# Performance work log

Measured on AMD Instinct MI355X. Metric: run time of the kernel, lower is better.

## Reference

```python
import jax, jax.numpy as jnp
import numpy as np

RNN = 50
FEAT = 128
NCLS = 8
ALPHA = 0.3  # keras LeakyReLU default


def setup_inputs() -> dict:
    key = jax.random.key(0)
    ks = jax.random.split(key, 6)
    B, T = 256, 2048
    x = jax.random.normal(ks[0], (B, T, FEAT), dtype=jnp.float32)
    # GRU params (Keras layout: kernel [F,3H], recurrent [H,3H], bias [2,3H] for reset_after=True)
    W = jax.random.normal(ks[1], (FEAT, 3 * RNN), dtype=jnp.float32) / np.sqrt(FEAT)
    U = jax.random.normal(ks[2], (RNN, 3 * RNN), dtype=jnp.float32) / np.sqrt(RNN)
    b = jax.random.normal(ks[3], (2, 3 * RNN), dtype=jnp.float32) * 0.01
    W2 = jax.random.normal(ks[4], (RNN, NCLS), dtype=jnp.float32) / np.sqrt(RNN)
    b2 = jnp.zeros((NCLS,), dtype=jnp.float32)
    return {"inputs": x, "W": W, "U": U, "b": b, "W2": W2, "b2": b2}


def _gru_last_state(x, W, U, b):
    # x: [B,T,F] -> precompute input projections [T,B,3H]
    B = x.shape[0]
    xw = jnp.einsum("btf,fh->tbh", x, W) + b[0]
    h0 = jnp.zeros((B, RNN), dtype=x.dtype)

    def step(h, xt):
        inner = h @ U + b[1]                       # [B,3H]
        z = jax.nn.sigmoid(xt[:, :RNN] + inner[:, :RNN])
        r = jax.nn.sigmoid(xt[:, RNN:2 * RNN] + inner[:, RNN:2 * RNN])
        hh = jnp.tanh(xt[:, 2 * RNN:] + r * inner[:, 2 * RNN:])
        h_new = z * h + (1.0 - z) * hh
        return h_new, None

    h_last, _ = jax.lax.scan(step, h0, xw)
    return h_last  # [B,H]


def reference(inputs, W, U, b, W2, b2):
    h = _gru_last_state(inputs, W, U, b)
    h = jnp.where(h >= 0, h, ALPHA * h)            # LeakyReLU(0.3)
    logits = h @ W2 + b2
    return jax.nn.softmax(logits, axis=-1)
```

## Files before the change

kernel.cpp:

```cpp
#include <hip/hip_runtime.h>

typedef __attribute__((ext_vector_type(4))) float f32x4;
typedef _Float16 f16;
typedef __attribute__((ext_vector_type(2))) _Float16 f16x2;
typedef __attribute__((ext_vector_type(8))) _Float16 f16x8;

#define T_LEN 2048
#define B_SZ 256
#define FEATN 128
#define H 50
#define H3 150
#define XW_STRIDE 160

__device__ __forceinline__ float rcpf(float x) { return __builtin_amdgcn_rcpf(x); }

__device__ __forceinline__ float dot2f(f16x2 a, f16x2 b, float c) {
  return __builtin_amdgcn_fdot2(a, b, c, false);
}

__global__ __launch_bounds__(256) void xw_gemm(const float* __restrict__ x,
                                               const float* __restrict__ W,
                                               f16* __restrict__ xw) {
  __shared__ f16 Wt[160 * 136];
  const int tid = threadIdx.x;
  for (int idx = tid; idx < FEATN * H3; idx += 256) {
    int f = idx / H3;
    int n = idx - f * H3;
    Wt[n * 136 + f] = (f16)W[idx];
  }
  for (int idx = tid; idx < 10 * FEATN; idx += 256) {
    int n = H3 + (idx >> 7);
    int f = idx & 127;
    Wt[n * 136 + f] = (f16)0.f;
  }
  __syncthreads();

  const int wid = tid >> 6;
  const int lane = tid & 63;
  const int l15 = lane & 15;
  const int g = lane >> 4;
  const long row0 = (long)blockIdx.x * 128 + wid * 32;

  f16x8 a[2][4];
#pragma unroll
  for (int sub = 0; sub < 2; ++sub) {
    const float* xp = x + (row0 + sub * 16 + l15) * FEATN + g * 8;
#pragma unroll
    for (int kk = 0; kk < 4; ++kk) {
      f32x4 p0 = *(const f32x4*)(xp + kk * 32);
      f32x4 p1 = *(const f32x4*)(xp + kk * 32 + 4);
      f16x8 v;
      v[0] = (f16)p0[0]; v[1] = (f16)p0[1]; v[2] = (f16)p0[2]; v[3] = (f16)p0[3];
      v[4] = (f16)p1[0]; v[5] = (f16)p1[1]; v[6] = (f16)p1[2]; v[7] = (f16)p1[3];
      a[sub][kk] = v;
    }
  }

  for (int nt = 0; nt < 10; ++nt) {
    const f16* bp = &Wt[(nt * 16 + l15) * 136 + g * 8];
    f16x8 bf0 = *(const f16x8*)(bp);
    f16x8 bf1 = *(const f16x8*)(bp + 32);
    f16x8 bf2 = *(const f16x8*)(bp + 64);
    f16x8 bf3 = *(const f16x8*)(bp + 96);
    f32x4 acc0 = {0.f, 0.f, 0.f, 0.f};
    f32x4 acc1 = {0.f, 0.f, 0.f, 0.f};
    acc0 = __builtin_amdgcn_mfma_f32_16x16x32_f16(a[0][0], bf0, acc0, 0, 0, 0);
    acc0 = __builtin_amdgcn_mfma_f32_16x16x32_f16(a[0][1], bf1, acc0, 0, 0, 0);
    acc0 = __builtin_amdgcn_mfma_f32_16x16x32_f16(a[0][2], bf2, acc0, 0, 0, 0);
    acc0 = __builtin_amdgcn_mfma_f32_16x16x32_f16(a[0][3], bf3, acc0, 0, 0, 0);
    acc1 = __builtin_amdgcn_mfma_f32_16x16x32_f16(a[1][0], bf0, acc1, 0, 0, 0);
    acc1 = __builtin_amdgcn_mfma_f32_16x16x32_f16(a[1][1], bf1, acc1, 0, 0, 0);
    acc1 = __builtin_amdgcn_mfma_f32_16x16x32_f16(a[1][2], bf2, acc1, 0, 0, 0);
    acc1 = __builtin_amdgcn_mfma_f32_16x16x32_f16(a[1][3], bf3, acc1, 0, 0, 0);
    int col = nt * 16 + l15;
    if (col < H3) {
#pragma unroll
      for (int r = 0; r < 4; ++r) {
        long rowA = row0 + g * 4 + r;
        xw[rowA * XW_STRIDE + col] = (f16)acc0[r];
        xw[(rowA + 16) * XW_STRIDE + col] = (f16)acc1[r];
      }
    }
  }
}

__global__ __launch_bounds__(64, 1) void gru_head64(const f16* __restrict__ xw,
                                                    const float* __restrict__ U,
                                                    const float* __restrict__ bias,
                                                    const float* __restrict__ W2,
                                                    const float* __restrict__ b2,
                                                    float* __restrict__ out) {
  __shared__ __align__(16) f16 h_lds16[64];
  __shared__ float fin[52];
  __shared__ float red[8];
  const int l = threadIdx.x;
  const int b = blockIdx.x;
  const int lc = l < H ? l : H - 1;
  const bool act = l < H;
  const long base = (long)b * T_LEN * XW_STRIDE;

  f16x2 uz2[25], ur2[25], uh2[25];
#pragma unroll
  for (int c = 0; c < 25; ++c) {
    uz2[c][0] = (f16)U[(2 * c) * H3 + lc];
    uz2[c][1] = (f16)U[(2 * c + 1) * H3 + lc];
    ur2[c][0] = (f16)U[(2 * c) * H3 + H + lc];
    ur2[c][1] = (f16)U[(2 * c + 1) * H3 + H + lc];
    uh2[c][0] = (f16)U[(2 * c) * H3 + 2 * H + lc];
    uh2[c][1] = (f16)U[(2 * c + 1) * H3 + 2 * H + lc];
  }
  const float bz = bias[lc] + bias[H3 + lc];
  const float br = bias[H + lc] + bias[H3 + H + lc];
  const float b0h = bias[2 * H + lc];
  const float b1h = bias[H3 + 2 * H + lc];

  float hreg = 0.f;
  h_lds16[l] = (f16)0.f;

  const f16* q = xw + base + lc;
  f16 pz[4], pr[4], ph[4];
#pragma unroll
  for (int p = 0; p < 4; ++p) {
    pz[p] = q[p * XW_STRIDE];
    pr[p] = q[p * XW_STRIDE + H];
    ph[p] = q[p * XW_STRIDE + 2 * H];
  }

  const f16x8* hp8 = (const f16x8*)h_lds16;

#define STEP(P, PF)                                                           \
    {                                                                         \
           \
      f16x8 w0 = hp8[0], w1 = hp8[1], w2 = hp8[2];                            \
      f16x8 w3 = hp8[3], w4 = hp8[4], w5 = hp8[5];                            \
      f16x2 w6 = *(const f16x2*)(h_lds16 + 48);                               \
               \
      float xzf = (float)pz[P];                                               \
      float xrf = (float)pr[P];                                               \
      float xhf = (float)ph[P];                                               \
      if (PF) {                                                               \
        pz[P] = q[(P + 4) * XW_STRIDE];                                       \
        pr[P] = q[(P + 4) * XW_STRIDE + H];                                   \
        ph[P] = q[(P + 4) * XW_STRIDE + 2 * H];                               \
      }                                                                       \
      f16x2 hv[25];                                                           \
      hv[0] = __builtin_shufflevector(w0, w0, 0, 1);                          \
      hv[1] = __builtin_shufflevector(w0, w0, 2, 3);                          \
      hv[2] = __builtin_shufflevector(w0, w0, 4, 5);                          \
      hv[3] = __builtin_shufflevector(w0, w0, 6, 7);                          \
      hv[4] = __builtin_shufflevector(w1, w1, 0, 1);                          \
      hv[5] = __builtin_shufflevector(w1, w1, 2, 3);                          \
      hv[6] = __builtin_shufflevector(w1, w1, 4, 5);                          \
      hv[7] = __builtin_shufflevector(w1, w1, 6, 7);                          \
      hv[8] = __builtin_shufflevector(w2, w2, 0, 1);                          \
      hv[9] = __builtin_shufflevector(w2, w2, 2, 3);                          \
      hv[10] = __builtin_shufflevector(w2, w2, 4, 5);                         \
      hv[11] = __builtin_shufflevector(w2, w2, 6, 7);                         \
      hv[12] = __builtin_shufflevector(w3, w3, 0, 1);                         \
      hv[13] = __builtin_shufflevector(w3, w3, 2, 3);                         \
      hv[14] = __builtin_shufflevector(w3, w3, 4, 5);                         \
      hv[15] = __builtin_shufflevector(w3, w3, 6, 7);                         \
      hv[16] = __builtin_shufflevector(w4, w4, 0, 1);                         \
      hv[17] = __builtin_shufflevector(w4, w4, 2, 3);                         \
      hv[18] = __builtin_shufflevector(w4, w4, 4, 5);                         \
      hv[19] = __builtin_shufflevector(w4, w4, 6, 7);                         \
      hv[20] = __builtin_shufflevector(w5, w5, 0, 1);                         \
      hv[21] = __builtin_shufflevector(w5, w5, 2, 3);                         \
      hv[22] = __builtin_shufflevector(w5, w5, 4, 5);                         \
      hv[23] = __builtin_shufflevector(w5, w5, 6, 7);                         \
      hv[24] = w6;                                                            \
      float sz0 = bz, sr0 = br, sh0 = b1h;                                    \
      float sz1 = 0.f, sr1 = 0.f, sh1 = 0.f;                                  \
      _Pragma("unroll")                                                       \
      for (int p = 0; p < 25; ++p) {                                          \
        if (p & 1) {                                                          \
          sz1 = dot2f(hv[p], uz2[p], sz1);                                    \
          sr1 = dot2f(hv[p], ur2[p], sr1);                                    \
          sh1 = dot2f(hv[p], uh2[p], sh1);                                    \
        } else {                                                              \
          sz0 = dot2f(hv[p], uz2[p], sz0);                                    \
          sr0 = dot2f(hv[p], ur2[p], sr0);                                    \
          sh0 = dot2f(hv[p], uh2[p], sh0);                                    \
        }                                                                     \
      }                                                                       \
      float ar = (sr0 + sr1) + xrf;                                           \
      float er = __expf(-ar);                                                 \
      float az = (sz0 + sz1) + xzf;                                           \
      float ez = __expf(-az);                                                 \
      float rr = rcpf(1.f + er);                                              \
      float zz = rcpf(1.f + ez);                                              \
      float ah = fmaf(rr, sh0 + sh1, xhf + b0h);                              \
      float eh = __expf(-2.f * ah);                                           \
      float th = fmaf(2.f, rcpf(1.f + eh), -1.f);                             \
      hreg = fmaf(zz, hreg - th, th);                                         \
      h_lds16[l] = (f16)hreg;                                                 \
    }

  for (int t0 = 0; t0 < T_LEN - 4; t0 += 4) {
    STEP(0, 1) STEP(1, 1) STEP(2, 1) STEP(3, 1)
    q += 4 * XW_STRIDE;
  }
  STEP(0, 0) STEP(1, 0) STEP(2, 0) STEP(3, 0)
#undef STEP

  if (act) {
    fin[l] = hreg >= 0.f ? hreg : 0.3f * hreg;
  }
  if (l < 8) {
    float acc = b2[l];
#pragma unroll
    for (int j = 0; j < H; ++j) acc = fmaf(fin[j], W2[j * 8 + l], acc);
    red[l] = acc;
  }
  if (l < 8) {
    float m = red[0];
#pragma unroll
    for (int i = 1; i < 8; ++i) m = fmaxf(m, red[i]);
    float s = 0.f;
#pragma unroll
    for (int i = 0; i < 8; ++i) s += __expf(red[i] - m);
    out[b * 8 + l] = __expf(red[l] - m) / s;
  }
}

extern "C" void kernel_launch(void* const* d_in, const int* in_sizes, int n_in,
                              void* d_out, int out_size, void* d_ws, size_t ws_size,
                              hipStream_t stream) {
  const float* x = (const float*)d_in[0];
  const float* W = (const float*)d_in[1];
  const float* U = (const float*)d_in[2];
  const float* bias = (const float*)d_in[3];
  const float* W2 = (const float*)d_in[4];
  const float* b2 = (const float*)d_in[5];
  float* out = (float*)d_out;
  f16* xw = (f16*)d_ws;

  xw_gemm<<<4096, 256, 0, stream>>>(x, W, xw);
  gru_head64<<<256, 64, 0, stream>>>(xw, U, bias, W2, b2, out);
}
```

Measured before the change: 640.7 us.

## Split GRU gate computation across three waves with LDS barrier exchange

The recurrent kernel now runs three waves per batch row, each computing one gate's recurrent dot products (z, r, candidate) instead of one wave computing all three. The z and r gates are passed through LDS to the candidate wave, which updates the hidden state and publishes it for the next step. This shortens the serial per-step dot-product chain, at the cost of two workgroup barriers and extra LDS traffic per timestep.

```diff
diff --git a/kernel.cpp b/kernel.cpp
--- a/kernel.cpp
+++ b/kernel.cpp
@@ -11,6 +11,8 @@
 #define H 50
 #define H3 150
 #define XW_STRIDE 160
+
+#define SFENCE __builtin_amdgcn_sched_barrier(0)
 
 __device__ __forceinline__ float rcpf(float x) { return __builtin_amdgcn_rcpf(x); }
 
@@ -84,65 +86,58 @@
   }
 }
 
-__global__ __launch_bounds__(64, 1) void gru_head64(const f16* __restrict__ xw,
-                                                    const float* __restrict__ U,
-                                                    const float* __restrict__ bias,
-                                                    const float* __restrict__ W2,
-                                                    const float* __restrict__ b2,
-                                                    float* __restrict__ out) {
-  __shared__ __align__(16) f16 h_lds16[64];
+__global__ __launch_bounds__(192, 1) void gru3(const f16* __restrict__ xw,
+                                               const float* __restrict__ U,
+                                               const float* __restrict__ bias,
+                                               const float* __restrict__ W2,
+                                               const float* __restrict__ b2,
+                                               float* __restrict__ out) {
+  __shared__ __align__(16) f16 h16[64];
+  __shared__ float zbuf[64];
+  __shared__ float rbuf[64];
   __shared__ float fin[52];
   __shared__ float red[8];
-  const int l = threadIdx.x;
+  const int tid = threadIdx.x;
+  const int l = tid & 63;
+  const int wv = tid >> 6;
   const int b = blockIdx.x;
   const int lc = l < H ? l : H - 1;
   const bool act = l < H;
   const long base = (long)b * T_LEN * XW_STRIDE;
-
-  f16x2 uz2[25], ur2[25], uh2[25];
+  const int goff = wv * H;
+
+  f16x2 u2[25];
 #pragma unroll
   for (int c = 0; c < 25; ++c) {
-    uz2[c][0] = (f16)U[(2 * c) * H3 + lc];
-    uz2[c][1] = (f16)U[(2 * c + 1) * H3 + lc];
-    ur2[c][0] = (f16)U[(2 * c) * H3 + H + lc];
-    ur2[c][1] = (f16)U[(2 * c + 1) * H3 + H + lc];
-    uh2[c][0] = (f16)U[(2 * c) * H3 + 2 * H + lc];
-    uh2[c][1] = (f16)U[(2 * c + 1) * H3 + 2 * H + lc];
-  }
-  const float bz = bias[lc] + bias[H3 + lc];
-  const float br = bias[H + lc] + bias[H3 + H + lc];
+    u2[c][0] = (f16)U[(2 * c) * H3 + goff + lc];
+    u2[c][1] = (f16)U[(2 * c + 1) * H3 + goff + lc];
+  }
   const float b0h = bias[2 * H + lc];
-  const float b1h = bias[H3 + 2 * H + lc];
-
-  float hreg = 0.f;
-  h_lds16[l] = (f16)0.f;
-
-  const f16* q = xw + base + lc;
-  f16 pz[4], pr[4], ph[4];
-#pragma unroll
-  for (int p = 0; p < 4; ++p) {
-    pz[p] = q[p * XW_STRIDE];
-    pr[p] = q[p * XW_STRIDE + H];
-    ph[p] = q[p * XW_STRIDE + 2 * H];
-  }
-
-  const f16x8* hp8 = (const f16x8*)h_lds16;
+  const float bsum = (wv == 2) ? bias[H3 + 2 * H + lc]
+                               : bias[goff + lc] + bias[H3 + goff + lc];
+
+  float hold = 0.f;
+  h16[l] = (f16)0.f;
+
+  const f16* q = xw + base + goff + lc;
+  f16 px[4];
+#pragma unroll
+  for (int p = 0; p < 4; ++p) px[p] = q[p * XW_STRIDE];
+
+  SFENCE;
+  asm volatile("s_waitcnt lgkmcnt(0)");
+  SFENCE;
+  __builtin_amdgcn_s_barrier();
+
+  const f16x8* hp8 = (const f16x8*)h16;
 
 #define STEP(P, PF)                                                           \
     {                                                                         \
-           \
       f16x8 w0 = hp8[0], w1 = hp8[1], w2 = hp8[2];                            \
       f16x8 w3 = hp8[3], w4 = hp8[4], w5 = hp8[5];                            \
-      f16x2 w6 = *(const f16x2*)(h_lds16 + 48);                               \
-               \
-      float xzf = (float)pz[P];                                               \
-      float xrf = (float)pr[P];                                               \
-      float xhf = (float)ph[P];                                               \
-      if (PF) {                                                               \
-        pz[P] = q[(P + 4) * XW_STRIDE];                                       \
-        pr[P] = q[(P + 4) * XW_STRIDE + H];                                   \
-        ph[P] = q[(P + 4) * XW_STRIDE + 2 * H];                               \
-      }                                                                       \
+      f16x2 w6 = *(const f16x2*)(h16 + 48);                                   \
+      float xv = (float)px[P];                                                \
+      if (PF) px[P] = q[(P + 4) * XW_STRIDE];                                 \
       f16x2 hv[25];                                                           \
       hv[0] = __builtin_shufflevector(w0, w0, 0, 1);                          \
       hv[1] = __builtin_shufflevector(w0, w0, 2, 3);                          \
@@ -169,31 +164,39 @@
       hv[22] = __builtin_shufflevector(w5, w5, 4, 5);                         \
       hv[23] = __builtin_shufflevector(w5, w5, 6, 7);                         \
       hv[24] = w6;                                                            \
-      float sz0 = bz, sr0 = br, sh0 = b1h;                                    \
-      float sz1 = 0.f, sr1 = 0.f, sh1 = 0.f;                                  \
+      float s0 = bsum, s1 = 0.f;                                              \
       _Pragma("unroll")                                                       \
       for (int p = 0; p < 25; ++p) {                                          \
-        if (p & 1) {                                                          \
-          sz1 = dot2f(hv[p], uz2[p], sz1);                                    \
-          sr1 = dot2f(hv[p], ur2[p], sr1);                                    \
-          sh1 = dot2f(hv[p], uh2[p], sh1);                                    \
-        } else {                                                              \
-          sz0 = dot2f(hv[p], uz2[p], sz0);                                    \
-          sr0 = dot2f(hv[p], ur2[p], sr0);                                    \
-          sh0 = dot2f(hv[p], uh2[p], sh0);                                    \
-        }                                                                     \
+        if (p & 1) s1 = dot2f(hv[p], u2[p], s1);                              \
+        else s0 = dot2f(hv[p], u2[p], s0);                                    \
       }                                                                       \
-      float ar = (sr0 + sr1) + xrf;                                           \
-      float er = __expf(-ar);                                                 \
-      float az = (sz0 + sz1) + xzf;                                           \
-      float ez = __expf(-az);                                                 \
-      float rr = rcpf(1.f + er);                                              \
-      float zz = rcpf(1.f + ez);                                              \
-      float ah = fmaf(rr, sh0 + sh1, xhf + b0h);                              \
-      float eh = __expf(-2.f * ah);                                           \
-      float th = fmaf(2.f, rcpf(1.f + eh), -1.f);                             \
-      hreg = fmaf(zz, hreg - th, th);                                         \
-      h_lds16[l] = (f16)hreg;                                                 \
+      float s = s0 + s1;                                                      \
+      if (wv == 2) {                                                          \
+        float xhb = xv + b0h;                                                 \
+        SFENCE;                                                               \
+        __builtin_amdgcn_s_barrier();                  \
+        float zz = zbuf[l];                                                   \
+        float rr = rbuf[l];                                                   \
+        float ah = fmaf(rr, s, xhb);                                          \
+        float eh = __expf(-2.f * ah);                                         \
+        float th = fmaf(2.f, rcpf(1.f + eh), -1.f);                           \
+        hold = fmaf(zz, hold - th, th);                                       \
+        h16[l] = (f16)hold;                                                   \
+        SFENCE;                                                               \
+        asm volatile("s_waitcnt lgkmcnt(0)");                                 \
+        SFENCE;                                                               \
+        __builtin_amdgcn_s_barrier();                      \
+      } else {                                                                \
+        float a = s + xv;                                                     \
+        float g = rcpf(1.f + __expf(-a));                                     \
+        if (wv == 0) zbuf[l] = g;                                             \
+        else rbuf[l] = g;                                                     \
+        SFENCE;                                                               \
+        asm volatile("s_waitcnt lgkmcnt(0)");                                 \
+        SFENCE;                                                               \
+        __builtin_amdgcn_s_barrier();                               \
+        __builtin_amdgcn_s_barrier();                               \
+      }                                                                       \
     }
 
   for (int t0 = 0; t0 < T_LEN - 4; t0 += 4) {
@@ -203,23 +206,25 @@
   STEP(0, 0) STEP(1, 0) STEP(2, 0) STEP(3, 0)
 #undef STEP
 
-  if (act) {
-    fin[l] = hreg >= 0.f ? hreg : 0.3f * hreg;
-  }
-  if (l < 8) {
-    float acc = b2[l];
-#pragma unroll
-    for (int j = 0; j < H; ++j) acc = fmaf(fin[j], W2[j * 8 + l], acc);
-    red[l] = acc;
-  }
-  if (l < 8) {
-    float m = red[0];
-#pragma unroll
-    for (int i = 1; i < 8; ++i) m = fmaxf(m, red[i]);
-    float s = 0.f;
-#pragma unroll
-    for (int i = 0; i < 8; ++i) s += __expf(red[i] - m);
-    out[b * 8 + l] = __expf(red[l] - m) / s;
+  if (wv == 2) {
+    if (act) {
+      fin[l] = hold >= 0.f ? hold : 0.3f * hold;
+    }
+    if (l < 8) {
+      float acc = b2[l];
+#pragma unroll
+      for (int j = 0; j < H; ++j) acc = fmaf(fin[j], W2[j * 8 + l], acc);
+      red[l] = acc;
+    }
+    if (l < 8) {
+      float m = red[0];
+#pragma unroll
+      for (int i = 1; i < 8; ++i) m = fmaxf(m, red[i]);
+      float s = 0.f;
+#pragma unroll
+      for (int i = 0; i < 8; ++i) s += __expf(red[i] - m);
+      out[b * 8 + l] = __expf(red[l] - m) / s;
+    }
   }
 }
 
@@ -236,5 +241,5 @@
   f16* xw = (f16*)d_ws;
 
   xw_gemm<<<4096, 256, 0, stream>>>(x, W, xw);
-  gru_head64<<<256, 64, 0, stream>>>(xw, U, bias, W2, b2, out);
-}
+  gru3<<<256, 192, 0, stream>>>(xw, U, bias, W2, b2, out);
+}
```

After: 741.1 us. +15.7%, slower.
